# Optimization experiments

Measured on AMD Instinct MI355X. Metric: run time of the kernel, lower is better.

The kernel has to match this reference:

```python
import jax, jax.numpy as jnp
import numpy as np

HIDDEN = 768
HEADS = 12
HEAD_DIM = HIDDEN // HEADS
INTER = 1152
WINDOW = 128
EPS = 1e-5
ROPE_WAVELENGTH = 10000.0


def setup_inputs() -> dict:
    key = jax.random.key(0)
    ks = jax.random.split(key, 8)
    B, S = 2, 2048
    x = jax.random.normal(ks[0], (B, S, HIDDEN), dtype=jnp.float32)
    padding_mask = jnp.ones((B, S), dtype=jnp.int32)
    sc = 0.02
    wqkv = jax.random.normal(ks[1], (HIDDEN, 3 * HIDDEN), dtype=jnp.float32) * sc
    wo_attn = jax.random.normal(ks[2], (HIDDEN, HIDDEN), dtype=jnp.float32) * sc
    wi0 = jax.random.normal(ks[3], (HIDDEN, INTER), dtype=jnp.float32) * sc
    wi1 = jax.random.normal(ks[4], (HIDDEN, INTER), dtype=jnp.float32) * sc
    wo_mlp = jax.random.normal(ks[5], (INTER, HIDDEN), dtype=jnp.float32) * sc
    g_attn = jnp.ones((HIDDEN,), dtype=jnp.float32)
    g_mlp = jnp.ones((HIDDEN,), dtype=jnp.float32)
    return dict(x=x, padding_mask=padding_mask, wqkv=wqkv, wo_attn=wo_attn,
                wi0=wi0, wi1=wi1, wo_mlp=wo_mlp, g_attn=g_attn, g_mlp=g_mlp)


def _rmsnorm(x, gamma):
    # Keras LayerNormalization(rms_scaling=True): x * rsqrt(mean(x^2)+eps) * gamma
    inv = jax.lax.rsqrt(jnp.mean(jnp.square(x), axis=-1, keepdims=True) + EPS)
    return x * inv * gamma


def _rope(t):
    # t: [B, S, H, D]; standard rotate-half RoPE over the head dim
    S, D = t.shape[1], t.shape[3]
    inv_freq = 1.0 / (ROPE_WAVELENGTH ** (jnp.arange(0, D, 2, dtype=jnp.float32) / D))
    freqs = jnp.arange(S, dtype=jnp.float32)[:, None] * inv_freq[None, :]  # [S, D/2]
    emb = jnp.concatenate([freqs, freqs], axis=-1)  # [S, D]
    cos = jnp.cos(emb)[None, :, None, :]
    sin = jnp.sin(emb)[None, :, None, :]
    h1, h2 = jnp.split(t, 2, axis=-1)
    rot = jnp.concatenate([-h2, h1], axis=-1)
    return t * cos + rot * sin


def reference(x, padding_mask, wqkv, wo_attn, wi0, wi1, wo_mlp, g_attn, g_mlp):
    B, S, _ = x.shape
    # --- attention sub-block ---
    res = x
    h = _rmsnorm(x, g_attn)
    qkv = (h @ wqkv).reshape(B, S, 3, HEADS, HEAD_DIM)
    q, k, v = qkv[:, :, 0], qkv[:, :, 1], qkv[:, :, 2]  # [B, S, H, D]
    q = _rope(q)
    k = _rope(k)
    scores = jnp.einsum('bqhd,bkhd->bhqk', q, k) / jnp.sqrt(
        jnp.asarray(HEAD_DIM, x.dtype))
    pos = jnp.arange(S)
    window = (jnp.abs(pos[:, None] - pos[None, :]) <= WINDOW // 2).astype(jnp.float32)
    mask = window[None, None, :, :] * padding_mask.astype(jnp.float32)[:, None, None, :]
    scores = scores + (1.0 - mask) * -1e9
    attn = jax.nn.softmax(scores, axis=-1)
    out = jnp.einsum('bhqk,bkhd->bqhd', attn, v).reshape(B, S, HIDDEN)
    x = res + out @ wo_attn
    # --- GeGLU MLP sub-block ---
    res = x
    h = _rmsnorm(x, g_mlp)
    h = jax.nn.gelu(h @ wi0, approximate=True) * (h @ wi1)
    return res + h @ wo_mlp
```

## Files before the change

### kernel.cpp

```cpp
#include <hip/hip_runtime.h>
#include <hip/hip_bf16.h>

#define HID 768
#define NHEADS 12
#define HD 64
#define INTER 1152
#define SEQ 2048
#define NB 2
#define ROWS (NB * SEQ)
#define QTA 64
#define KTA 192

typedef __attribute__((ext_vector_type(8))) short bf16x8;
typedef __attribute__((ext_vector_type(4))) float f32x4;

__device__ __forceinline__ unsigned short f2bf(float f) {
    union { float f; unsigned int i; } c; c.f = f;
    unsigned int b = c.i;
    b += 0x7FFFu + ((b >> 16) & 1u);
    return (unsigned short)(b >> 16);
}
__device__ __forceinline__ void gload16(const void* g, void* l) {
    __builtin_amdgcn_global_load_lds((const __attribute__((address_space(1))) unsigned int*)g,
                                     (__attribute__((address_space(3))) unsigned int*)l,
                                     16, 0, 0);
}

__device__ __forceinline__ void wt_tile(const float* __restrict__ W,
                                        unsigned short* __restrict__ Wt,
                                        int K, int N, int bx, int by,
                                        float (*t)[33]) {
    int tx = threadIdx.x & 31, ty = threadIdx.x >> 5;
    #pragma unroll
    for (int i = 0; i < 4; ++i)
        t[ty + i * 8][tx] = W[(size_t)(by * 32 + ty + i * 8) * N + bx * 32 + tx];
    __syncthreads();
    #pragma unroll
    for (int i = 0; i < 4; ++i)
        Wt[(size_t)(bx * 32 + ty + i * 8) * K + by * 32 + tx] = f2bf(t[tx][ty + i * 8]);
}

__global__ __launch_bounds__(256) void prep_rms_kernel(const float* __restrict__ x,
                                                       const float* __restrict__ g,
                                                       unsigned short* __restrict__ hbf,
                                                       const float* __restrict__ wqkv,
                                                       const float* __restrict__ woa,
                                                       const float* __restrict__ wi0,
                                                       const float* __restrict__ wi1,
                                                       const float* __restrict__ wom,
                                                       unsigned short* __restrict__ wqkvT,
                                                       unsigned short* __restrict__ woaT,
                                                       unsigned short* __restrict__ wi0T,
                                                       unsigned short* __restrict__ wi1T,
                                                       unsigned short* __restrict__ womT,
                                                       float2* __restrict__ rtab) {
    __shared__ float t[32][33];
    __shared__ float red[4];
    int id = blockIdx.x;
    int tid = threadIdx.x;
    if (id < 4096) {
        const float* xr = x + (size_t)id * HID;
        unsigned short* orow = hbf + (size_t)id * HID;
        float v0 = xr[tid], v1 = xr[tid + 256], v2 = xr[tid + 512];
        float s = v0 * v0 + v1 * v1 + v2 * v2;
        #pragma unroll
        for (int m = 32; m >= 1; m >>= 1) s += __shfl_xor(s, m, 64);
        if ((tid & 63) == 0) red[tid >> 6] = s;
        __syncthreads();
        float tot = red[0] + red[1] + red[2] + red[3];
        float inv = rsqrtf(tot * (1.0f / HID) + 1e-5f);
        orow[tid]       = f2bf(v0 * inv * g[tid]);
        orow[tid + 256] = f2bf(v1 * inv * g[tid + 256]);
        orow[tid + 512] = f2bf(v2 * inv * g[tid + 512]);
        return;
    }
    id -= 4096;
    if (id < 1728)       wt_tile(wqkv, wqkvT, 768, 2304, id % 72, id / 72, t);
    else if (id < 2304)  { id -= 1728; wt_tile(woa, woaT, 768, 768, id % 24, id / 24, t); }
    else if (id < 3168)  { id -= 2304; wt_tile(wi0, wi0T, 768, 1152, id % 36, id / 36, t); }
    else if (id < 4032)  { id -= 3168; wt_tile(wi1, wi1T, 768, 1152, id % 36, id / 36, t); }
    else if (id < 4896)  { id -= 4032; wt_tile(wom, womT, 1152, 768, id % 24, id / 24, t); }
    else {
        int idx = (id - 4896) * 256 + tid;
        int s = idx >> 5, fi = idx & 31;
        float ang = (float)s * exp2f(-(float)fi * 0.41524101186f);
        float sn, cs;
        sincosf(ang, &sn, &cs);
        rtab[idx] = make_float2(cs, sn);
    }
}

__global__ __launch_bounds__(256) void rmsnorm_kernel(const float* __restrict__ x,
                                                      const float* __restrict__ g,
                                                      unsigned short* __restrict__ out) {
    int row = blockIdx.x;
    const float* xr = x + (size_t)row * HID;
    unsigned short* orow = out + (size_t)row * HID;
    int tid = threadIdx.x;
    float v0 = xr[tid], v1 = xr[tid + 256], v2 = xr[tid + 512];
    float s = v0 * v0 + v1 * v1 + v2 * v2;
    #pragma unroll
    for (int m = 32; m >= 1; m >>= 1) s += __shfl_xor(s, m, 64);
    __shared__ float red[4];
    if ((tid & 63) == 0) red[tid >> 6] = s;
    __syncthreads();
    float tot = red[0] + red[1] + red[2] + red[3];
    float inv = rsqrtf(tot * (1.0f / HID) + 1e-5f);
    orow[tid]       = f2bf(v0 * inv * g[tid]);
    orow[tid + 256] = f2bf(v1 * inv * g[tid + 256]);
    orow[tid + 512] = f2bf(v2 * inv * g[tid + 512]);
}

__global__ __launch_bounds__(256) void gemm_wo128(const unsigned short* __restrict__ A,
                                                  const unsigned short* __restrict__ Bt,
                                                  const float* __restrict__ resid,
                                                  float* __restrict__ C,
                                                  int N, int K) {
    __shared__ unsigned short As[128 * 128];
    __shared__ unsigned short Bs[64 * 128];
    int nbx = N >> 6;
    int nwg = gridDim.x;
    int bid = blockIdx.x;
    int id2 = (bid & 7) * (nwg >> 3) + (bid >> 3);
    int col0 = (id2 % nbx) * 64, row0 = (id2 / nbx) * 128;
    int tid = threadIdx.x;
    int wave = tid >> 6, lane = tid & 63;
    int fr = lane & 15, fq = lane >> 4;

    const size_t strideA = (size_t)K * 2;
    const char* Ab = (const char*)A;
    const char* Bb = (const char*)Bt;

    f32x4 acc[2][4];
    #pragma unroll
    for (int m = 0; m < 2; ++m)
        #pragma unroll
        for (int n = 0; n < 4; ++n)
            acc[m][n] = (f32x4){0.f, 0.f, 0.f, 0.f};

    int nt = K >> 7;
    for (int t = 0; t < nt; ++t) {
        int k0 = t << 7;
        #pragma unroll
        for (int r = 0; r < 8; ++r) {
            int L = r * 4096 + tid * 16;
            int row = L >> 8;
            int ss = ((L >> 4) & 15) ^ (row & 15);
            gload16(Ab + (size_t)(row0 + row) * strideA + (size_t)k0 * 2 + ss * 16,
                    (char*)As + L);
        }
        #pragma unroll
        for (int r = 0; r < 4; ++r) {
            int L = r * 4096 + tid * 16;
            int row = L >> 8;
            int ss = ((L >> 4) & 15) ^ (row & 15);
            gload16(Bb + (size_t)(col0 + row) * strideA + (size_t)k0 * 2 + ss * 16,
                    (char*)Bs + L);
        }
        __syncthreads();
        #pragma unroll
        for (int kk = 0; kk < 4; ++kk) {
            bf16x8 af[2], bf[4];
            #pragma unroll
            for (int m = 0; m < 2; ++m) {
                int rowa = wave * 32 + m * 16 + fr;
                af[m] = *(const bf16x8*)&As[rowa * 128 + ((kk * 4 + fq) ^ (rowa & 15)) * 8];
            }
            #pragma unroll
            for (int n = 0; n < 4; ++n) {
                int rowb = n * 16 + fr;
                bf[n] = *(const bf16x8*)&Bs[rowb * 128 + ((kk * 4 + fq) ^ (rowb & 15)) * 8];
            }
            #pragma unroll
            for (int m = 0; m < 2; ++m)
                #pragma unroll
                for (int n = 0; n < 4; ++n)
                    acc[m][n] = __builtin_amdgcn_mfma_f32_16x16x32_bf16(af[m], bf[n], acc[m][n], 0, 0, 0);
        }
        __syncthreads();
    }

    #pragma unroll
    for (int m = 0; m < 2; ++m)
        #pragma unroll
        for (int j = 0; j < 4; ++j) {
            size_t r = (size_t)(row0 + wave * 32 + m * 16 + fq * 4 + j);
            #pragma unroll
            for (int n = 0; n < 4; ++n) {
                size_t idx = r * N + (col0 + n * 16 + fr);
                C[idx] = acc[m][n][j] + resid[idx];
            }
        }
}

__global__ __launch_bounds__(256) void gemm_qkv128(const unsigned short* __restrict__ A,
                                                   const unsigned short* __restrict__ Bt,
                                                   const float2* __restrict__ rtab,
                                                   unsigned short* __restrict__ Qb,
                                                   unsigned short* __restrict__ Kb,
                                                   unsigned short* __restrict__ Vt) {
    __shared__ unsigned short As[128 * 128];
    __shared__ unsigned short Bs[64 * 128];
    int bid = blockIdx.x;
    int id2 = (bid & 7) * 144 + (bid >> 3);
    int col0 = (id2 % 36) * 64, row0 = (id2 / 36) * 128;
    int tid = threadIdx.x;
    int wave = tid >> 6, lane = tid & 63;
    int fr = lane & 15, fq = lane >> 4;
    int type = col0 / 768;
    int h = (col0 % 768) >> 6;
    int b = row0 >> 11;
    int s0 = row0 & 2047;
    int bh = b * NHEADS + h;

    const size_t strideA = (size_t)768 * 2;
    const char* Ab = (const char*)A;
    const char* Bb = (const char*)Bt;

    f32x4 acc[2][4];
    #pragma unroll
    for (int m = 0; m < 2; ++m)
        #pragma unroll
        for (int n = 0; n < 4; ++n)
            acc[m][n] = (f32x4){0.f, 0.f, 0.f, 0.f};

    for (int t = 0; t < 6; ++t) {
        int k0 = t << 7;
        #pragma unroll
        for (int r = 0; r < 8; ++r) {
            int L = r * 4096 + tid * 16;
            int row = L >> 8;
            int ss = ((L >> 4) & 15) ^ (row & 15);
            gload16(Ab + (size_t)(row0 + row) * strideA + (size_t)k0 * 2 + ss * 16,
                    (char*)As + L);
        }
        #pragma unroll
        for (int r = 0; r < 4; ++r) {
            int L = r * 4096 + tid * 16;
            int row = L >> 8;
            int ss = ((L >> 4) & 15) ^ (row & 15);
            gload16(Bb + (size_t)(col0 + row) * strideA + (size_t)k0 * 2 + ss * 16,
                    (char*)Bs + L);
        }
        __syncthreads();
        #pragma unroll
        for (int kk = 0; kk < 4; ++kk) {
            bf16x8 af[2], bf[4];
            #pragma unroll
            for (int m = 0; m < 2; ++m) {
                int rowa = wave * 32 + m * 16 + fr;
                af[m] = *(const bf16x8*)&As[rowa * 128 + ((kk * 4 + fq) ^ (rowa & 15)) * 8];
            }
            #pragma unroll
            for (int n = 0; n < 4; ++n) {
                int rowb = n * 16 + fr;
                bf[n] = *(const bf16x8*)&Bs[rowb * 128 + ((kk * 4 + fq) ^ (rowb & 15)) * 8];
            }
            #pragma unroll
            for (int m = 0; m < 2; ++m)
                #pragma unroll
                for (int n = 0; n < 4; ++n)
                    acc[m][n] = __builtin_amdgcn_mfma_f32_16x16x32_bf16(af[m], bf[n], acc[m][n], 0, 0, 0);
        }
        __syncthreads();
    }

    if (type < 2) {
        unsigned short* P = (type == 0 ? Qb : Kb) + ((size_t)bh * SEQ) * 64;
        #pragma unroll
        for (int m = 0; m < 2; ++m)
            #pragma unroll
            for (int n = 0; n < 4; ++n) {
                int d = n * 16 + fr;
                int fi = d & 31;
                #pragma unroll
                for (int j = 0; j < 4; ++j) {
                    int s = s0 + wave * 32 + m * 16 + fq * 4 + j;
                    float2 cs = rtab[s * 32 + fi];
                    float val = acc[m][n][j], par = acc[m][n ^ 2][j];
                    float o = (d < 32) ? val * cs.x - par * cs.y
                                       : val * cs.x + par * cs.y;
                    P[(size_t)s * 64 + d] = f2bf(o);
                }
            }
    } else {
        unsigned short* vt = As;
        #pragma unroll
        for (int m = 0; m < 2; ++m)
            #pragma unroll
            for (int n = 0; n < 4; ++n) {
                int d = n * 16 + fr;
                #pragma unroll
                for (int j = 0; j < 4; ++j)
                    vt[d * 136 + wave * 32 + m * 16 + fq * 4 + j] = f2bf(acc[m][n][j]);
            }
        __syncthreads();
        int d = tid >> 2, sg = tid & 3;
        unsigned short* vrow = Vt + ((size_t)bh * 64 + d) * SEQ + s0 + sg * 32;
        #pragma unroll
        for (int i = 0; i < 4; ++i)
            *(bf16x8*)(vrow + i * 8) = *(const bf16x8*)&vt[d * 136 + sg * 32 + i * 8];
    }
}

__global__ __launch_bounds__(256) void gemm_ffn128(const unsigned short* __restrict__ A,
                                                   const unsigned short* __restrict__ B0t,
                                                   const unsigned short* __restrict__ B1t,
                                                   unsigned short* __restrict__ O) {
    __shared__ unsigned short As[128 * 64];
    __shared__ unsigned short Bs0[64 * 64];
    __shared__ unsigned short Bs1[64 * 64];
    int bid = blockIdx.x;
    int id2 = (bid & 7) * 72 + (bid >> 3);
    int col0 = (id2 % 18) * 64, row0 = (id2 / 18) * 128;
    int tid = threadIdx.x;
    int wave = tid >> 6, lane = tid & 63;
    int fr = lane & 15, fq = lane >> 4;

    f32x4 acc0[2][4], acc1[2][4];
    #pragma unroll
    for (int m = 0; m < 2; ++m)
        #pragma unroll
        for (int n = 0; n < 4; ++n) {
            acc0[m][n] = (f32x4){0.f, 0.f, 0.f, 0.f};
            acc1[m][n] = (f32x4){0.f, 0.f, 0.f, 0.f};
        }

    const size_t strideA = (size_t)768 * 2;
    const char* Ab  = (const char*)A;
    const char* B0b = (const char*)B0t;
    const char* B1b = (const char*)B1t;

    for (int k0 = 0; k0 < 768; k0 += 64) {
        #pragma unroll
        for (int r = 0; r < 4; ++r) {
            int L = r * 4096 + tid * 16;
            int row = L >> 7;
            int ss = ((L >> 4) & 7) ^ (row & 7);
            gload16(Ab + (size_t)(row0 + row) * strideA + (size_t)k0 * 2 + ss * 16,
                    (char*)As + L);
        }
        #pragma unroll
        for (int r = 0; r < 2; ++r) {
            int L = r * 4096 + tid * 16;
            int row = L >> 7;
            int ss = ((L >> 4) & 7) ^ (row & 7);
            size_t goff = (size_t)(col0 + row) * strideA + (size_t)k0 * 2 + ss * 16;
            gload16(B0b + goff, (char*)Bs0 + L);
            gload16(B1b + goff, (char*)Bs1 + L);
        }
        __syncthreads();
        #pragma unroll
        for (int kk = 0; kk < 2; ++kk) {
            bf16x8 af[2], b0[4], b1[4];
            #pragma unroll
            for (int m = 0; m < 2; ++m) {
                int rowa = wave * 32 + m * 16 + fr;
                af[m] = *(const bf16x8*)&As[rowa * 64 + ((kk * 4 + fq) ^ (rowa & 7)) * 8];
            }
            #pragma unroll
            for (int n = 0; n < 4; ++n) {
                int rowb = n * 16 + fr;
                int sl = ((kk * 4 + fq) ^ (rowb & 7)) * 8;
                b0[n] = *(const bf16x8*)&Bs0[rowb * 64 + sl];
                b1[n] = *(const bf16x8*)&Bs1[rowb * 64 + sl];
            }
            #pragma unroll
            for (int m = 0; m < 2; ++m)
                #pragma unroll
                for (int n = 0; n < 4; ++n) {
                    acc0[m][n] = __builtin_amdgcn_mfma_f32_16x16x32_bf16(af[m], b0[n], acc0[m][n], 0, 0, 0);
                    acc1[m][n] = __builtin_amdgcn_mfma_f32_16x16x32_bf16(af[m], b1[n], acc1[m][n], 0, 0, 0);
                }
        }
        __syncthreads();
    }

    #pragma unroll
    for (int m = 0; m < 2; ++m)
        #pragma unroll
        for (int n = 0; n < 4; ++n)
            #pragma unroll
            for (int j = 0; j < 4; ++j) {
                int r = row0 + wave * 32 + m * 16 + fq * 4 + j;
                float xa = acc0[m][n][j];
                float tn = tanhf(0.7978845608028654f * (xa + 0.044715f * xa * xa * xa));
                float gv = 0.5f * xa * (1.f + tn) * acc1[m][n][j];
                O[(size_t)r * INTER + col0 + n * 16 + fr] = f2bf(gv);
            }
}

__global__ __launch_bounds__(256) void attn_mfma(const unsigned short* __restrict__ Qb,
                                                 const unsigned short* __restrict__ Kb,
                                                 const unsigned short* __restrict__ Vt,
                                                 const int* __restrict__ pmask,
                                                 unsigned short* __restrict__ ao) {
    __shared__ unsigned short Ks[KTA * 64];
    __shared__ unsigned short Vs[64 * KTA];
    __shared__ float pmsk[KTA];

    int bid = blockIdx.x;
    int qt = bid & 31;
    int h  = (bid >> 5) % NHEADS;
    int b  = bid / (32 * NHEADS);
    int bh = b * NHEADS + h;
    int q0 = qt * QTA;
    int kstart = q0 - 64;
    int tid = threadIdx.x;
    int wave = tid >> 6, lane = tid & 63;
    int fr = lane & 15, fq = lane >> 4;

    const unsigned short* Kg = Kb + ((size_t)bh * SEQ) * 64;
    const unsigned short* Vg = Vt + ((size_t)bh * 64) * SEQ;

    const unsigned short* Qg = Qb + ((size_t)bh * SEQ + q0 + wave * 16 + fr) * 64 + fq * 8;
    bf16x8 qf0 = *(const bf16x8*)(Qg);
    bf16x8 qf1 = *(const bf16x8*)(Qg + 32);
    if (tid < KTA) {
        int k = kstart + tid;
        pmsk[tid] = (k >= 0 && k < SEQ) ? (1.0f - (float)pmask[b * SEQ + k]) * -1e9f
                                        : -1e9f;
    }

    bool interior = (qt != 0) && (qt != 31);
    if (interior) {
        #pragma unroll
        for (int r = 0; r < 6; ++r) {
            int c = r * 256 + tid;
            int row = c >> 3, slot = c & 7;
            int ss = slot ^ (row & 7);
            gload16(Kg + (size_t)(kstart + row) * 64 + ss * 8, (char*)Ks + c * 16);
        }
        #pragma unroll
        for (int r = 0; r < 6; ++r) {
            int c = r * 256 + tid;
            int d = c / 24, slot = c - d * 24;
            int ss = (slot & ~7) | ((slot & 7) ^ (d & 7));
            gload16(Vg + (size_t)d * SEQ + kstart + ss * 8, (char*)Vs + c * 16);
        }
    } else {
        #pragma unroll
        for (int r = 0; r < 6; ++r) {
            int c = r * 256 + tid;
            int row = c >> 3, slot = c & 7;
            int ss = slot ^ (row & 7);
            int sk = kstart + row;
            bf16x8 val = {0, 0, 0, 0, 0, 0, 0, 0};
            if (sk >= 0 && sk < SEQ)
                val = *(const bf16x8*)(Kg + (size_t)sk * 64 + ss * 8);
            *(bf16x8*)((char*)Ks + c * 16) = val;
        }
        #pragma unroll
        for (int r = 0; r < 6; ++r) {
            int c = r * 256 + tid;
            int d = c / 24, slot = c - d * 24;
            int ss = (slot & ~7) | ((slot & 7) ^ (d & 7));
            int start = kstart + ss * 8;
            bf16x8 val = {0, 0, 0, 0, 0, 0, 0, 0};
            if (start >= 0 && start + 8 <= SEQ)
                val = *(const bf16x8*)(Vg + (size_t)d * SEQ + start);
            *(bf16x8*)((char*)Vs + c * 16) = val;
        }
    }
    __syncthreads();

    f32x4 sc[9];
    #pragma unroll
    for (int ni = 0; ni < 9; ++ni) sc[ni] = (f32x4){0.f, 0.f, 0.f, 0.f};
    #pragma unroll
    for (int ni = 0; ni < 9; ++ni) {
        int row = (wave + ni) * 16 + fr;
        int base = row * 64;
        bf16x8 k0 = *(const bf16x8*)&Ks[base + ((fq)     ^ (row & 7)) * 8];
        bf16x8 k1 = *(const bf16x8*)&Ks[base + ((4 + fq) ^ (row & 7)) * 8];
        sc[ni] = __builtin_amdgcn_mfma_f32_16x16x32_bf16(qf0, k0, sc[ni], 0, 0, 0);
        sc[ni] = __builtin_amdgcn_mfma_f32_16x16x32_bf16(qf1, k1, sc[ni], 0, 0, 0);
    }

    int qrow_base = q0 + wave * 16 + fq * 4;
    float mj[4] = {-1e30f, -1e30f, -1e30f, -1e30f}, sj[4];
    #pragma unroll
    for (int ni = 0; ni < 9; ++ni) {
        int kp = (wave + ni) * 16 + fr;
        int k = kstart + kp;
        float pm = pmsk[kp];
        #pragma unroll
        for (int j = 0; j < 4; ++j) {
            int diff = qrow_base + j - k;
            float s = sc[ni][j] * 0.125f + pm;
            if (diff > 64 || diff < -64) s = -1e30f;
            sc[ni][j] = s;
            mj[j] = fmaxf(mj[j], s);
        }
    }
    #pragma unroll
    for (int j = 0; j < 4; ++j) {
        #pragma unroll
        for (int mk = 1; mk < 16; mk <<= 1)
            mj[j] = fmaxf(mj[j], __shfl_xor(mj[j], mk, 16));
        sj[j] = 0.f;
    }
    #pragma unroll
    for (int ni = 0; ni < 9; ++ni)
        #pragma unroll
        for (int j = 0; j < 4; ++j) {
            float e = expf(sc[ni][j] - mj[j]);
            sc[ni][j] = e;
            sj[j] += e;
        }
    #pragma unroll
    for (int j = 0; j < 4; ++j)
        #pragma unroll
        for (int mk = 1; mk < 16; mk <<= 1)
            sj[j] += __shfl_xor(sj[j], mk, 16);

    __syncthreads();

    unsigned short* Pw = Ks + wave * 16 * KTA;
    #pragma unroll
    for (int ni = 0; ni < 9; ++ni) {
        int n = wave + ni;
        int slot = n * 2 + (fr >> 3);
        #pragma unroll
        for (int j = 0; j < 4; ++j) {
            int row = fq * 4 + j;
            int ss = (slot & ~7) | ((slot & 7) ^ (row & 7));
            Pw[row * KTA + ss * 8 + (fr & 7)] = f2bf(sc[ni][j]);
        }
    }
    #pragma unroll
    for (int n = 0; n < 12; ++n) {
        if (n >= wave && n <= wave + 8) continue;
        int slot = n * 2 + (fr >> 3);
        #pragma unroll
        for (int j = 0; j < 4; ++j) {
            int row = fq * 4 + j;
            int ss = (slot & ~7) | ((slot & 7) ^ (row & 7));
            Pw[row * KTA + ss * 8 + (fr & 7)] = 0;
        }
    }

    f32x4 oacc[4];
    #pragma unroll
    for (int n = 0; n < 4; ++n) oacc[n] = (f32x4){0.f, 0.f, 0.f, 0.f};
    int kt0 = wave >> 1;
    #pragma unroll
    for (int ki = 0; ki < 5; ++ki) {
        int slot = (kt0 + ki) * 4 + fq;
        int ssp = (slot & ~7) | ((slot & 7) ^ (fr & 7));
        bf16x8 pa = *(const bf16x8*)&Pw[fr * KTA + ssp * 8];
        #pragma unroll
        for (int n = 0; n < 4; ++n) {
            int d = n * 16 + fr;
            int ssv = (slot & ~7) | ((slot & 7) ^ (d & 7));
            bf16x8 vf = *(const bf16x8*)&Vs[d * KTA + ssv * 8];
            oacc[n] = __builtin_amdgcn_mfma_f32_16x16x32_bf16(pa, vf, oacc[n], 0, 0, 0);
        }
    }

    unsigned short* aob = ao + ((size_t)(b * SEQ + qrow_base)) * HID + h * 64;
    float rs[4];
    #pragma unroll
    for (int j = 0; j < 4; ++j) rs[j] = 1.0f / sj[j];
    #pragma unroll
    for (int n = 0; n < 4; ++n)
        #pragma unroll
        for (int j = 0; j < 4; ++j)
            aob[(size_t)j * HID + n * 16 + fr] = f2bf(oacc[n][j] * rs[j]);
}

extern "C" void kernel_launch(void* const* d_in, const int* in_sizes, int n_in,
                              void* d_out, int out_size, void* d_ws, size_t ws_size,
                              hipStream_t stream) {
    const float* x       = (const float*)d_in[0];
    const int*   pmask   = (const int*)d_in[1];
    const float* wqkv    = (const float*)d_in[2];
    const float* wo_attn = (const float*)d_in[3];
    const float* wi0     = (const float*)d_in[4];
    const float* wi1     = (const float*)d_in[5];
    const float* wo_mlp  = (const float*)d_in[6];
    const float* g_attn  = (const float*)d_in[7];
    const float* g_mlp   = (const float*)d_in[8];
    float* out = (float*)d_out;

    char* w = (char*)d_ws;
    unsigned short* hbf   = (unsigned short*)(w);
    unsigned short* aobf  = (unsigned short*)(w + 6291456);
    unsigned short* Qb    = (unsigned short*)(w + 12582912);
    unsigned short* Kb    = (unsigned short*)(w + 18874368);
    unsigned short* Vt    = (unsigned short*)(w + 25165824);
    unsigned short* mgate = (unsigned short*)(w + 31457280);
    float2*         rtab  = (float2*)(w + 40894464);
    unsigned short* wqkvT = (unsigned short*)(w + 41418752);
    unsigned short* woaT  = (unsigned short*)(w + 44957696);
    unsigned short* wi0T  = (unsigned short*)(w + 46137344);
    unsigned short* wi1T  = (unsigned short*)(w + 47906816);
    unsigned short* womT  = (unsigned short*)(w + 49676288);

    prep_rms_kernel<<<4096 + 5152, 256, 0, stream>>>(x, g_attn, hbf,
                                                     wqkv, wo_attn, wi0, wi1, wo_mlp,
                                                     wqkvT, woaT, wi0T, wi1T, womT, rtab);
    gemm_qkv128<<<1152, 256, 0, stream>>>(hbf, wqkvT, rtab, Qb, Kb, Vt);
    attn_mfma<<<NB * NHEADS * (SEQ / QTA), 256, 0, stream>>>(Qb, Kb, Vt, pmask, aobf);
    gemm_wo128<<<384, 256, 0, stream>>>(aobf, woaT, x, out, 768, 768);
    rmsnorm_kernel<<<ROWS, 256, 0, stream>>>(out, g_mlp, hbf);
    gemm_ffn128<<<576, 256, 0, stream>>>(hbf, wi0T, wi1T, mgate);
    gemm_wo128<<<384, 256, 0, stream>>>(mgate, womT, out, out, 768, 1152);
}
```

Measured before the change: 115.3 us.

## Use 128x128 2x2-wave tiles for QKV and interleaved-weight GeGLU GEMMs

```diff
diff --git a/kernel.cpp b/kernel.cpp
--- a/kernel.cpp
+++ b/kernel.cpp
@@ -38,6 +38,23 @@
     #pragma unroll
     for (int i = 0; i < 4; ++i)
         Wt[(size_t)(bx * 32 + ty + i * 8) * K + by * 32 + tx] = f2bf(t[tx][ty + i * 8]);
+}
+
+__device__ __forceinline__ void wt_tile_i(const float* __restrict__ W,
+                                          unsigned short* __restrict__ Wt,
+                                          int p, int bx, int by,
+                                          float (*t)[33]) {
+    int tx = threadIdx.x & 31, ty = threadIdx.x >> 5;
+    #pragma unroll
+    for (int i = 0; i < 4; ++i)
+        t[ty + i * 8][tx] = W[(size_t)(by * 32 + ty + i * 8) * INTER + bx * 32 + tx];
+    __syncthreads();
+    #pragma unroll
+    for (int i = 0; i < 4; ++i) {
+        int n = bx * 32 + ty + i * 8;
+        int ri = ((n >> 4) << 5) + p * 16 + (n & 15);
+        Wt[(size_t)ri * 768 + by * 32 + tx] = f2bf(t[tx][ty + i * 8]);
+    }
 }
 
 __global__ __launch_bounds__(256) void prep_rms_kernel(const float* __restrict__ x,
@@ -50,8 +67,7 @@
                                                        const float* __restrict__ wom,
                                                        unsigned short* __restrict__ wqkvT,
                                                        unsigned short* __restrict__ woaT,
-                                                       unsigned short* __restrict__ wi0T,
-                                                       unsigned short* __restrict__ wi1T,
+                                                       unsigned short* __restrict__ wiT,
                                                        unsigned short* __restrict__ womT,
                                                        float2* __restrict__ rtab) {
     __shared__ float t[32][33];
@@ -77,8 +93,8 @@
     id -= 4096;
     if (id < 1728)       wt_tile(wqkv, wqkvT, 768, 2304, id % 72, id / 72, t);
     else if (id < 2304)  { id -= 1728; wt_tile(woa, woaT, 768, 768, id % 24, id / 24, t); }
-    else if (id < 3168)  { id -= 2304; wt_tile(wi0, wi0T, 768, 1152, id % 36, id / 36, t); }
-    else if (id < 4032)  { id -= 3168; wt_tile(wi1, wi1T, 768, 1152, id % 36, id / 36, t); }
+    else if (id < 3168)  { id -= 2304; wt_tile_i(wi0, wiT, 0, id % 36, id / 36, t); }
+    else if (id < 4032)  { id -= 3168; wt_tile_i(wi1, wiT, 1, id % 36, id / 36, t); }
     else if (id < 4896)  { id -= 4032; wt_tile(wom, womT, 1152, 768, id % 24, id / 24, t); }
     else {
         int idx = (id - 4896) * 256 + tid;
@@ -193,71 +209,65 @@
         }
 }
 
-__global__ __launch_bounds__(256) void gemm_qkv128(const unsigned short* __restrict__ A,
-                                                   const unsigned short* __restrict__ Bt,
-                                                   const float2* __restrict__ rtab,
-                                                   unsigned short* __restrict__ Qb,
-                                                   unsigned short* __restrict__ Kb,
-                                                   unsigned short* __restrict__ Vt) {
-    __shared__ unsigned short As[128 * 128];
-    __shared__ unsigned short Bs[64 * 128];
+__global__ __launch_bounds__(256) void gemm_qkv(const unsigned short* __restrict__ A,
+                                                const unsigned short* __restrict__ Bt,
+                                                const float2* __restrict__ rtab,
+                                                unsigned short* __restrict__ Qb,
+                                                unsigned short* __restrict__ Kb,
+                                                unsigned short* __restrict__ Vt) {
+    __shared__ unsigned short As[128 * 64];
+    __shared__ unsigned short Bs[128 * 64];
     int bid = blockIdx.x;
-    int id2 = (bid & 7) * 144 + (bid >> 3);
-    int col0 = (id2 % 36) * 64, row0 = (id2 / 36) * 128;
+    int id2 = (bid & 7) * 72 + (bid >> 3);
+    int col0 = (id2 % 18) * 128, row0 = (id2 / 18) * 128;
     int tid = threadIdx.x;
     int wave = tid >> 6, lane = tid & 63;
+    int wr = wave >> 1, wc = wave & 1;
     int fr = lane & 15, fq = lane >> 4;
     int type = col0 / 768;
-    int h = (col0 % 768) >> 6;
+    int head2 = (col0 % 768) >> 6;
     int b = row0 >> 11;
     int s0 = row0 & 2047;
-    int bh = b * NHEADS + h;
 
     const size_t strideA = (size_t)768 * 2;
     const char* Ab = (const char*)A;
     const char* Bb = (const char*)Bt;
 
-    f32x4 acc[2][4];
-    #pragma unroll
-    for (int m = 0; m < 2; ++m)
+    f32x4 acc[4][4];
+    #pragma unroll
+    for (int m = 0; m < 4; ++m)
         #pragma unroll
         for (int n = 0; n < 4; ++n)
             acc[m][n] = (f32x4){0.f, 0.f, 0.f, 0.f};
 
-    for (int t = 0; t < 6; ++t) {
-        int k0 = t << 7;
-        #pragma unroll
-        for (int r = 0; r < 8; ++r) {
+    for (int t = 0; t < 12; ++t) {
+        int k0 = t << 6;
+        #pragma unroll
+        for (int r = 0; r < 4; ++r) {
             int L = r * 4096 + tid * 16;
-            int row = L >> 8;
-            int ss = ((L >> 4) & 15) ^ (row & 15);
+            int row = L >> 7;
+            int ss = ((L >> 4) & 7) ^ (row & 7);
             gload16(Ab + (size_t)(row0 + row) * strideA + (size_t)k0 * 2 + ss * 16,
                     (char*)As + L);
-        }
-        #pragma unroll
-        for (int r = 0; r < 4; ++r) {
-            int L = r * 4096 + tid * 16;
-            int row = L >> 8;
-            int ss = ((L >> 4) & 15) ^ (row & 15);
             gload16(Bb + (size_t)(col0 + row) * strideA + (size_t)k0 * 2 + ss * 16,
                     (char*)Bs + L);
         }
         __syncthreads();
         #pragma unroll
-        for (int kk = 0; kk < 4; ++kk) {
-            bf16x8 af[2], bf[4];
-            #pragma unroll
-            for (int m = 0; m < 2; ++m) {
-                int rowa = wave * 32 + m * 16 + fr;
-                af[m] = *(const bf16x8*)&As[rowa * 128 + ((kk * 4 + fq) ^ (rowa & 15)) * 8];
+        for (int kk = 0; kk < 2; ++kk) {
+            bf16x8 af[4], bf[4];
+            #pragma unroll
+            for (int m = 0; m < 4; ++m) {
+                int rowa = wr * 64 + m * 16 + fr;
+                af[m] = *(const bf16x8*)&As[rowa * 64 + ((kk * 4 + fq) ^ (rowa & 7)) * 8];
             }
             #pragma unroll
             for (int n = 0; n < 4; ++n) {
-                int rowb = n * 16 + fr;
-                bf[n] = *(const bf16x8*)&Bs[rowb * 128 + ((kk * 4 + fq) ^ (rowb & 15)) * 8];
-            }
-            #pragma unroll
-            for (int m = 0; m < 2; ++m)
+                int rowb = wc * 64 + n * 16 + fr;
+                bf[n] = *(const bf16x8*)&Bs[rowb * 64 + ((kk * 4 + fq) ^ (rowb & 7)) * 8];
+            }
+            #pragma unroll
+            for (int m = 0; m < 4; ++m)
                 #pragma unroll
                 for (int n = 0; n < 4; ++n)
                     acc[m][n] = __builtin_amdgcn_mfma_f32_16x16x32_bf16(af[m], bf[n], acc[m][n], 0, 0, 0);
@@ -266,16 +276,17 @@
     }
 
     if (type < 2) {
-        unsigned short* P = (type == 0 ? Qb : Kb) + ((size_t)bh * SEQ) * 64;
-        #pragma unroll
-        for (int m = 0; m < 2; ++m)
+        int head = head2 + wc;
+        unsigned short* P = (type == 0 ? Qb : Kb) + ((size_t)(b * NHEADS + head) * SEQ) * 64;
+        #pragma unroll
+        for (int m = 0; m < 4; ++m)
             #pragma unroll
             for (int n = 0; n < 4; ++n) {
                 int d = n * 16 + fr;
                 int fi = d & 31;
                 #pragma unroll
                 for (int j = 0; j < 4; ++j) {
-                    int s = s0 + wave * 32 + m * 16 + fq * 4 + j;
+                    int s = s0 + wr * 64 + m * 16 + fq * 4 + j;
                     float2 cs = rtab[s * 32 + fi];
                     float val = acc[m][n][j], par = acc[m][n ^ 2][j];
                     float o = (d < 32) ? val * cs.x - par * cs.y
@@ -286,52 +297,56 @@
     } else {
         unsigned short* vt = As;
         #pragma unroll
-        for (int m = 0; m < 2; ++m)
-            #pragma unroll
-            for (int n = 0; n < 4; ++n) {
-                int d = n * 16 + fr;
+        for (int hp = 0; hp < 2; ++hp) {
+            __syncthreads();
+            if (wc == hp) {
                 #pragma unroll
-                for (int j = 0; j < 4; ++j)
-                    vt[d * 136 + wave * 32 + m * 16 + fq * 4 + j] = f2bf(acc[m][n][j]);
-            }
-        __syncthreads();
-        int d = tid >> 2, sg = tid & 3;
-        unsigned short* vrow = Vt + ((size_t)bh * 64 + d) * SEQ + s0 + sg * 32;
-        #pragma unroll
-        for (int i = 0; i < 4; ++i)
-            *(bf16x8*)(vrow + i * 8) = *(const bf16x8*)&vt[d * 136 + sg * 32 + i * 8];
-    }
-}
-
-__global__ __launch_bounds__(256) void gemm_ffn128(const unsigned short* __restrict__ A,
-                                                   const unsigned short* __restrict__ B0t,
-                                                   const unsigned short* __restrict__ B1t,
-                                                   unsigned short* __restrict__ O) {
+                for (int m = 0; m < 4; ++m)
+                    #pragma unroll
+                    for (int n = 0; n < 4; ++n) {
+                        int d = n * 16 + fr;
+                        #pragma unroll
+                        for (int j = 0; j < 4; ++j)
+                            vt[d * 136 + wr * 64 + m * 16 + fq * 4 + j] = f2bf(acc[m][n][j]);
+                    }
+            }
+            __syncthreads();
+            int head = head2 + hp;
+            int d = tid >> 2, sg = tid & 3;
+            unsigned short* vrow = Vt + (((size_t)(b * NHEADS + head)) * 64 + d) * SEQ + s0 + sg * 32;
+            #pragma unroll
+            for (int i = 0; i < 4; ++i)
+                *(bf16x8*)(vrow + i * 8) = *(const bf16x8*)&vt[d * 136 + sg * 32 + i * 8];
+        }
+    }
+}
+
+__global__ __launch_bounds__(256) void gemm_ffn(const unsigned short* __restrict__ A,
+                                                const unsigned short* __restrict__ Bt,
+                                                unsigned short* __restrict__ O) {
     __shared__ unsigned short As[128 * 64];
-    __shared__ unsigned short Bs0[64 * 64];
-    __shared__ unsigned short Bs1[64 * 64];
+    __shared__ unsigned short Bs[128 * 64];
     int bid = blockIdx.x;
     int id2 = (bid & 7) * 72 + (bid >> 3);
-    int col0 = (id2 % 18) * 64, row0 = (id2 / 18) * 128;
+    int col0 = (id2 % 18) * 128, row0 = (id2 / 18) * 128;
     int tid = threadIdx.x;
     int wave = tid >> 6, lane = tid & 63;
+    int wr = wave >> 1, wc = wave & 1;
     int fr = lane & 15, fq = lane >> 4;
 
-    f32x4 acc0[2][4], acc1[2][4];
-    #pragma unroll
-    for (int m = 0; m < 2; ++m)
-        #pragma unroll
-        for (int n = 0; n < 4; ++n) {
-            acc0[m][n] = (f32x4){0.f, 0.f, 0.f, 0.f};
-            acc1[m][n] = (f32x4){0.f, 0.f, 0.f, 0.f};
-        }
-
     const size_t strideA = (size_t)768 * 2;
-    const char* Ab  = (const char*)A;
-    const char* B0b = (const char*)B0t;
-    const char* B1b = (const char*)B1t;
-
-    for (int k0 = 0; k0 < 768; k0 += 64) {
+    const char* Ab = (const char*)A;
+    const char* Bb = (const char*)Bt;
+
+    f32x4 acc[4][4];
+    #pragma unroll
+    for (int m = 0; m < 4; ++m)
+        #pragma unroll
+        for (int n = 0; n < 4; ++n)
+            acc[m][n] = (f32x4){0.f, 0.f, 0.f, 0.f};
+
+    for (int t = 0; t < 12; ++t) {
+        int k0 = t << 6;
         #pragma unroll
         for (int r = 0; r < 4; ++r) {
             int L = r * 4096 + tid * 16;
@@ -339,54 +354,44 @@
             int ss = ((L >> 4) & 7) ^ (row & 7);
             gload16(Ab + (size_t)(row0 + row) * strideA + (size_t)k0 * 2 + ss * 16,
                     (char*)As + L);
-        }
-        #pragma unroll
-        for (int r = 0; r < 2; ++r) {
-            int L = r * 4096 + tid * 16;
-            int row = L >> 7;
-            int ss = ((L >> 4) & 7) ^ (row & 7);
-            size_t goff = (size_t)(col0 + row) * strideA + (size_t)k0 * 2 + ss * 16;
-            gload16(B0b + goff, (char*)Bs0 + L);
-            gload16(B1b + goff, (char*)Bs1 + L);
+            gload16(Bb + (size_t)(col0 + row) * strideA + (size_t)k0 * 2 + ss * 16,
+                    (char*)Bs + L);
         }
         __syncthreads();
         #pragma unroll
         for (int kk = 0; kk < 2; ++kk) {
-            bf16x8 af[2], b0[4], b1[4];
-            #pragma unroll
-            for (int m = 0; m < 2; ++m) {
-                int rowa = wave * 32 + m * 16 + fr;
+            bf16x8 af[4], bf[4];
+            #pragma unroll
+            for (int m = 0; m < 4; ++m) {
+                int rowa = wr * 64 + m * 16 + fr;
                 af[m] = *(const bf16x8*)&As[rowa * 64 + ((kk * 4 + fq) ^ (rowa & 7)) * 8];
             }
             #pragma unroll
             for (int n = 0; n < 4; ++n) {
-                int rowb = n * 16 + fr;
-                int sl = ((kk * 4 + fq) ^ (rowb & 7)) * 8;
-                b0[n] = *(const bf16x8*)&Bs0[rowb * 64 + sl];
-                b1[n] = *(const bf16x8*)&Bs1[rowb * 64 + sl];
-            }
-            #pragma unroll
-            for (int m = 0; m < 2; ++m)
+                int rowb = wc * 64 + n * 16 + fr;
+                bf[n] = *(const bf16x8*)&Bs[rowb * 64 + ((kk * 4 + fq) ^ (rowb & 7)) * 8];
+            }
+            #pragma unroll
+            for (int m = 0; m < 4; ++m)
                 #pragma unroll
-                for (int n = 0; n < 4; ++n) {
-                    acc0[m][n] = __builtin_amdgcn_mfma_f32_16x16x32_bf16(af[m], b0[n], acc0[m][n], 0, 0, 0);
-                    acc1[m][n] = __builtin_amdgcn_mfma_f32_16x16x32_bf16(af[m], b1[n], acc1[m][n], 0, 0, 0);
-                }
+                for (int n = 0; n < 4; ++n)
+                    acc[m][n] = __builtin_amdgcn_mfma_f32_16x16x32_bf16(af[m], bf[n], acc[m][n], 0, 0, 0);
         }
         __syncthreads();
     }
 
     #pragma unroll
-    for (int m = 0; m < 2; ++m)
-        #pragma unroll
-        for (int n = 0; n < 4; ++n)
+    for (int m = 0; m < 4; ++m)
+        #pragma unroll
+        for (int nl = 0; nl < 4; nl += 2)
             #pragma unroll
             for (int j = 0; j < 4; ++j) {
-                int r = row0 + wave * 32 + m * 16 + fq * 4 + j;
-                float xa = acc0[m][n][j];
+                int r = row0 + wr * 64 + m * 16 + fq * 4 + j;
+                float xa = acc[m][nl][j];
                 float tn = tanhf(0.7978845608028654f * (xa + 0.044715f * xa * xa * xa));
-                float gv = 0.5f * xa * (1.f + tn) * acc1[m][n][j];
-                O[(size_t)r * INTER + col0 + n * 16 + fr] = f2bf(gv);
+                float gv = 0.5f * xa * (1.f + tn) * acc[m][nl + 1][j];
+                int col = (col0 >> 1) + wc * 32 + (nl >> 1) * 16 + fr;
+                O[(size_t)r * INTER + col] = f2bf(gv);
             }
 }
 
@@ -593,17 +598,16 @@
     float2*         rtab  = (float2*)(w + 40894464);
     unsigned short* wqkvT = (unsigned short*)(w + 41418752);
     unsigned short* woaT  = (unsigned short*)(w + 44957696);
-    unsigned short* wi0T  = (unsigned short*)(w + 46137344);
-    unsigned short* wi1T  = (unsigned short*)(w + 47906816);
+    unsigned short* wiT   = (unsigned short*)(w + 46137344);
     unsigned short* womT  = (unsigned short*)(w + 49676288);
 
     prep_rms_kernel<<<4096 + 5152, 256, 0, stream>>>(x, g_attn, hbf,
                                                      wqkv, wo_attn, wi0, wi1, wo_mlp,
-                                                     wqkvT, woaT, wi0T, wi1T, womT, rtab);
-    gemm_qkv128<<<1152, 256, 0, stream>>>(hbf, wqkvT, rtab, Qb, Kb, Vt);
+                                                     wqkvT, woaT, wiT, womT, rtab);
+    gemm_qkv<<<576, 256, 0, stream>>>(hbf, wqkvT, rtab, Qb, Kb, Vt);
     attn_mfma<<<NB * NHEADS * (SEQ / QTA), 256, 0, stream>>>(Qb, Kb, Vt, pmask, aobf);
     gemm_wo128<<<384, 256, 0, stream>>>(aobf, woaT, x, out, 768, 768);
     rmsnorm_kernel<<<ROWS, 256, 0, stream>>>(out, g_mlp, hbf);
-    gemm_ffn128<<<576, 256, 0, stream>>>(hbf, wi0T, wi1T, mgate);
+    gemm_ffn<<<576, 256, 0, stream>>>(hbf, wiT, mgate);
     gemm_wo128<<<384, 256, 0, stream>>>(mgate, womT, out, out, 768, 1152);
 }
```

Measured after the change: 150.1 us. 30.2% more time.

## Interleave GeGLU weights into one matrix and deepen FFN GEMM K-tile

Applied to the files above, without the earlier changes.

```diff
diff --git a/kernel.cpp b/kernel.cpp
--- a/kernel.cpp
+++ b/kernel.cpp
@@ -38,6 +38,23 @@
     #pragma unroll
     for (int i = 0; i < 4; ++i)
         Wt[(size_t)(bx * 32 + ty + i * 8) * K + by * 32 + tx] = f2bf(t[tx][ty + i * 8]);
+}
+
+__device__ __forceinline__ void wt_tile_i(const float* __restrict__ W,
+                                          unsigned short* __restrict__ Wt,
+                                          int p, int bx, int by,
+                                          float (*t)[33]) {
+    int tx = threadIdx.x & 31, ty = threadIdx.x >> 5;
+    #pragma unroll
+    for (int i = 0; i < 4; ++i)
+        t[ty + i * 8][tx] = W[(size_t)(by * 32 + ty + i * 8) * INTER + bx * 32 + tx];
+    __syncthreads();
+    #pragma unroll
+    for (int i = 0; i < 4; ++i) {
+        int n = bx * 32 + ty + i * 8;
+        int ri = ((n >> 4) << 5) + p * 16 + (n & 15);
+        Wt[(size_t)ri * 768 + by * 32 + tx] = f2bf(t[tx][ty + i * 8]);
+    }
 }
 
 __global__ __launch_bounds__(256) void prep_rms_kernel(const float* __restrict__ x,
@@ -50,8 +67,7 @@
                                                        const float* __restrict__ wom,
                                                        unsigned short* __restrict__ wqkvT,
                                                        unsigned short* __restrict__ woaT,
-                                                       unsigned short* __restrict__ wi0T,
-                                                       unsigned short* __restrict__ wi1T,
+                                                       unsigned short* __restrict__ wiT,
                                                        unsigned short* __restrict__ womT,
                                                        float2* __restrict__ rtab) {
     __shared__ float t[32][33];
@@ -77,8 +93,8 @@
     id -= 4096;
     if (id < 1728)       wt_tile(wqkv, wqkvT, 768, 2304, id % 72, id / 72, t);
     else if (id < 2304)  { id -= 1728; wt_tile(woa, woaT, 768, 768, id % 24, id / 24, t); }
-    else if (id < 3168)  { id -= 2304; wt_tile(wi0, wi0T, 768, 1152, id % 36, id / 36, t); }
-    else if (id < 4032)  { id -= 3168; wt_tile(wi1, wi1T, 768, 1152, id % 36, id / 36, t); }
+    else if (id < 3168)  { id -= 2304; wt_tile_i(wi0, wiT, 0, id % 36, id / 36, t); }
+    else if (id < 4032)  { id -= 3168; wt_tile_i(wi1, wiT, 1, id % 36, id / 36, t); }
     else if (id < 4896)  { id -= 4032; wt_tile(wom, womT, 1152, 768, id % 24, id / 24, t); }
     else {
         int idx = (id - 4896) * 256 + tid;
@@ -303,75 +319,66 @@
     }
 }
 
-__global__ __launch_bounds__(256) void gemm_ffn128(const unsigned short* __restrict__ A,
-                                                   const unsigned short* __restrict__ B0t,
-                                                   const unsigned short* __restrict__ B1t,
-                                                   unsigned short* __restrict__ O) {
-    __shared__ unsigned short As[128 * 64];
-    __shared__ unsigned short Bs0[64 * 64];
-    __shared__ unsigned short Bs1[64 * 64];
+__global__ __launch_bounds__(256) void gemm_ffn128i(const unsigned short* __restrict__ A,
+                                                    const unsigned short* __restrict__ Bt,
+                                                    unsigned short* __restrict__ O) {
+    __shared__ unsigned short As[128 * 128];
+    __shared__ unsigned short Bs[64 * 128];
     int bid = blockIdx.x;
-    int id2 = (bid & 7) * 72 + (bid >> 3);
-    int col0 = (id2 % 18) * 64, row0 = (id2 / 18) * 128;
+    int id2 = (bid & 7) * 144 + (bid >> 3);
+    int col0 = (id2 % 36) * 64, row0 = (id2 / 36) * 128;
     int tid = threadIdx.x;
     int wave = tid >> 6, lane = tid & 63;
     int fr = lane & 15, fq = lane >> 4;
 
-    f32x4 acc0[2][4], acc1[2][4];
+    const size_t strideA = (size_t)768 * 2;
+    const char* Ab = (const char*)A;
+    const char* Bb = (const char*)Bt;
+
+    f32x4 acc[2][4];
     #pragma unroll
     for (int m = 0; m < 2; ++m)
         #pragma unroll
-        for (int n = 0; n < 4; ++n) {
-            acc0[m][n] = (f32x4){0.f, 0.f, 0.f, 0.f};
-            acc1[m][n] = (f32x4){0.f, 0.f, 0.f, 0.f};
-        }
-
-    const size_t strideA = (size_t)768 * 2;
-    const char* Ab  = (const char*)A;
-    const char* B0b = (const char*)B0t;
-    const char* B1b = (const char*)B1t;
-
-    for (int k0 = 0; k0 < 768; k0 += 64) {
+        for (int n = 0; n < 4; ++n)
+            acc[m][n] = (f32x4){0.f, 0.f, 0.f, 0.f};
+
+    for (int t = 0; t < 6; ++t) {
+        int k0 = t << 7;
+        #pragma unroll
+        for (int r = 0; r < 8; ++r) {
+            int L = r * 4096 + tid * 16;
+            int row = L >> 8;
+            int ss = ((L >> 4) & 15) ^ (row & 15);
+            gload16(Ab + (size_t)(row0 + row) * strideA + (size_t)k0 * 2 + ss * 16,
+                    (char*)As + L);
+        }
         #pragma unroll
         for (int r = 0; r < 4; ++r) {
             int L = r * 4096 + tid * 16;
-            int row = L >> 7;
-            int ss = ((L >> 4) & 7) ^ (row & 7);
-            gload16(Ab + (size_t)(row0 + row) * strideA + (size_t)k0 * 2 + ss * 16,
-                    (char*)As + L);
-        }
-        #pragma unroll
-        for (int r = 0; r < 2; ++r) {
-            int L = r * 4096 + tid * 16;
-            int row = L >> 7;
-            int ss = ((L >> 4) & 7) ^ (row & 7);
-            size_t goff = (size_t)(col0 + row) * strideA + (size_t)k0 * 2 + ss * 16;
-            gload16(B0b + goff, (char*)Bs0 + L);
-            gload16(B1b + goff, (char*)Bs1 + L);
-        }
-        __syncthreads();
-        #pragma unroll
-        for (int kk = 0; kk < 2; ++kk) {
-            bf16x8 af[2], b0[4], b1[4];
+            int row = L >> 8;
+            int ss = ((L >> 4) & 15) ^ (row & 15);
+            gload16(Bb + (size_t)(col0 + row) * strideA + (size_t)k0 * 2 + ss * 16,
+                    (char*)Bs + L);
+        }
+        __syncthreads();
+        #pragma unroll
+        for (int kk = 0; kk < 4; ++kk) {
+            bf16x8 af[2], bf[4];
             #pragma unroll
             for (int m = 0; m < 2; ++m) {
                 int rowa = wave * 32 + m * 16 + fr;
-                af[m] = *(const bf16x8*)&As[rowa * 64 + ((kk * 4 + fq) ^ (rowa & 7)) * 8];
+                af[m] = *(const bf16x8*)&As[rowa * 128 + ((kk * 4 + fq) ^ (rowa & 15)) * 8];
             }
             #pragma unroll
             for (int n = 0; n < 4; ++n) {
                 int rowb = n * 16 + fr;
-                int sl = ((kk * 4 + fq) ^ (rowb & 7)) * 8;
-                b0[n] = *(const bf16x8*)&Bs0[rowb * 64 + sl];
-                b1[n] = *(const bf16x8*)&Bs1[rowb * 64 + sl];
+                bf[n] = *(const bf16x8*)&Bs[rowb * 128 + ((kk * 4 + fq) ^ (rowb & 15)) * 8];
             }
             #pragma unroll
             for (int m = 0; m < 2; ++m)
                 #pragma unroll
-                for (int n = 0; n < 4; ++n) {
-                    acc0[m][n] = __builtin_amdgcn_mfma_f32_16x16x32_bf16(af[m], b0[n], acc0[m][n], 0, 0, 0);
-                    acc1[m][n] = __builtin_amdgcn_mfma_f32_16x16x32_bf16(af[m], b1[n], acc1[m][n], 0, 0, 0);
-                }
+                for (int n = 0; n < 4; ++n)
+                    acc[m][n] = __builtin_amdgcn_mfma_f32_16x16x32_bf16(af[m], bf[n], acc[m][n], 0, 0, 0);
         }
         __syncthreads();
     }
@@ -379,14 +386,15 @@
     #pragma unroll
     for (int m = 0; m < 2; ++m)
         #pragma unroll
-        for (int n = 0; n < 4; ++n)
+        for (int np = 0; np < 4; np += 2)
             #pragma unroll
             for (int j = 0; j < 4; ++j) {
                 int r = row0 + wave * 32 + m * 16 + fq * 4 + j;
-                float xa = acc0[m][n][j];
+                float xa = acc[m][np][j];
                 float tn = tanhf(0.7978845608028654f * (xa + 0.044715f * xa * xa * xa));
-                float gv = 0.5f * xa * (1.f + tn) * acc1[m][n][j];
-                O[(size_t)r * INTER + col0 + n * 16 + fr] = f2bf(gv);
+                float gv = 0.5f * xa * (1.f + tn) * acc[m][np + 1][j];
+                int col = (col0 >> 1) + (np >> 1) * 16 + fr;
+                O[(size_t)r * INTER + col] = f2bf(gv);
             }
 }
 
@@ -400,9 +408,10 @@
     __shared__ float pmsk[KTA];
 
     int bid = blockIdx.x;
-    int qt = bid & 31;
-    int h  = (bid >> 5) % NHEADS;
-    int b  = bid / (32 * NHEADS);
+    int id2 = (bid & 7) * 96 + (bid >> 3);
+    int qt = id2 & 31;
+    int h  = (id2 >> 5) % NHEADS;
+    int b  = id2 / (32 * NHEADS);
     int bh = b * NHEADS + h;
     int q0 = qt * QTA;
     int kstart = q0 - 64;
@@ -593,17 +602,16 @@
     float2*         rtab  = (float2*)(w + 40894464);
     unsigned short* wqkvT = (unsigned short*)(w + 41418752);
     unsigned short* woaT  = (unsigned short*)(w + 44957696);
-    unsigned short* wi0T  = (unsigned short*)(w + 46137344);
-    unsigned short* wi1T  = (unsigned short*)(w + 47906816);
+    unsigned short* wiT   = (unsigned short*)(w + 46137344);
     unsigned short* womT  = (unsigned short*)(w + 49676288);
 
     prep_rms_kernel<<<4096 + 5152, 256, 0, stream>>>(x, g_attn, hbf,
                                                      wqkv, wo_attn, wi0, wi1, wo_mlp,
-                                                     wqkvT, woaT, wi0T, wi1T, womT, rtab);
+                                                     wqkvT, woaT, wiT, womT, rtab);
     gemm_qkv128<<<1152, 256, 0, stream>>>(hbf, wqkvT, rtab, Qb, Kb, Vt);
     attn_mfma<<<NB * NHEADS * (SEQ / QTA), 256, 0, stream>>>(Qb, Kb, Vt, pmask, aobf);
     gemm_wo128<<<384, 256, 0, stream>>>(aobf, woaT, x, out, 768, 768);
     rmsnorm_kernel<<<ROWS, 256, 0, stream>>>(out, g_mlp, hbf);
-    gemm_ffn128<<<576, 256, 0, stream>>>(hbf, wi0T, wi1T, mgate);
+    gemm_ffn128i<<<1152, 256, 0, stream>>>(hbf, wiT, mgate);
     gemm_wo128<<<384, 256, 0, stream>>>(mgate, womT, out, out, 768, 1152);
 }
```

Result: no change. 114.0 us (-1.1%).
